# Kernel optimization log

Hardware: AMD Instinct MI355X
Metric: run time of the kernel (lower is better)

The kernel has to match this reference:

```python
import jax, jax.numpy as jnp
import numpy as np

LN_EPS = 1e-5

def setup_inputs() -> dict:
    key = jax.random.key(0)
    ks = jax.random.split(key, 6)
    N, CD, CC, CF = 500000, 64, 96, 128
    return {
        "x_detial": jax.random.normal(ks[0], (N, CD), dtype=jnp.float32),
        "x_context": jax.random.normal(ks[1], (N, CC), dtype=jnp.float32),
        "W_detial": jax.random.normal(ks[2], (CD, CF), dtype=jnp.float32) * 0.05,
        "W_context": jax.random.normal(ks[3], (CC, CF), dtype=jnp.float32) * 0.05,
        "W_gate1": jax.random.normal(ks[4], (CD + CC, CF // 2), dtype=jnp.float32) * 0.05,
        "ln_gamma": jnp.ones((CF // 2,), dtype=jnp.float32),
        "ln_beta": jnp.zeros((CF // 2,), dtype=jnp.float32),
        "W_gate2": jax.random.normal(ks[5], (CF // 2, 1), dtype=jnp.float32) * 0.05,
    }

def _layer_norm(x, gamma, beta):
    mu = jnp.mean(x, axis=-1, keepdims=True)
    var = jnp.mean(jnp.square(x - mu), axis=-1, keepdims=True)
    return (x - mu) * jax.lax.rsqrt(var + LN_EPS) * gamma + beta

def reference(x_detial, x_context, W_detial, W_context, W_gate1, ln_gamma, ln_beta, W_gate2):
    # gate path: 1x1 subm conv == per-point linear on [N, C] features
    concat = jnp.concatenate([x_detial, x_context], axis=1)        # [N, CD+CC]
    h = jnp.matmul(concat, W_gate1)                                 # [N, CF//2]
    h = jax.nn.relu(_layer_norm(h, ln_gamma, ln_beta))
    gate = jax.nn.sigmoid(jnp.matmul(h, W_gate2))                   # [N, 1]
    detail_aligned = jnp.matmul(x_detial, W_detial)                 # [N, CF]
    context_aligned = jnp.matmul(x_context, W_context)              # [N, CF]
    return (1.0 - gate) * context_aligned + gate * detail_aligned   # [N, CF]
```

## Files before the change

kernel.cpp:

```cpp
#include <hip/hip_runtime.h>
#include <hip/hip_bf16.h>
#include <math.h>


namespace {

typedef __attribute__((ext_vector_type(8))) short short8;
typedef __attribute__((ext_vector_type(4))) float f32x4;

constexpr int CD = 64, CC = 96, CH = 64, CF = 128;
constexpr int NFG1 = 20;
constexpr int NFCB = 40;
constexpr int NFRAG = NFG1 + NFCB;
constexpr int WCHUNKS = NFCB * 512 * 2 / 16;

__device__ inline short bf16_of(float f) {
  __hip_bfloat16 h = __float2bfloat16(f);
  return *reinterpret_cast<short*>(&h);
}

__global__ void convert_weights(const float* __restrict__ Wd,
                                const float* __restrict__ Wc,
                                const float* __restrict__ Wg1,
                                short* __restrict__ ws) {
  const int t = blockIdx.x * 256 + threadIdx.x;
  if (t >= 64 * NFRAG) return;
  const int frag = t >> 6, l = t & 63;
  const int cidx = l & 15, kb = l >> 4;
  float v[8];
  if (frag < NFG1) {
    const int ks = frag >> 2, nt = frag & 3;
    const int n = nt * 16 + cidx;
    #pragma unroll
    for (int j = 0; j < 8; ++j) {
      const int k = ks * 32 + (j >> 2) * 16 + kb * 4 + (j & 3);
      v[j] = Wg1[k * CH + n];
    }
  } else {
    const int f2 = frag - NFG1;
    const int ks = f2 >> 3, nt = f2 & 7;
    const int n = nt * 16 + cidx;
    #pragma unroll
    for (int j = 0; j < 8; ++j) {
      const int k = ks * 32 + (j >> 2) * 16 + kb * 4 + (j & 3);
      v[j] = (k < CD) ? Wd[k * CF + n] : Wc[(k - CD) * CF + n];
    }
  }
  short8 o;
  #pragma unroll
  for (int j = 0; j < 8; ++j) o[j] = bf16_of(v[j]);
  *reinterpret_cast<short8*>(ws + frag * 512 + l * 8) = o;
}

__global__ __launch_bounds__(512, 4)
void gate_fusion_mfma(const float* __restrict__ xd,
                      const float* __restrict__ xc,
                      const float* __restrict__ gma,
                      const float* __restrict__ bta,
                      const float* __restrict__ Wg2,
                      const short* __restrict__ wf,
                      float* __restrict__ out, int N) {
  __shared__ short wlds[NFCB * 512];

  const int tid  = threadIdx.x;
  const int lane = tid & 63;
  const int wv   = tid >> 6;
  const int r0   = blockIdx.x * 128 + wv * 16;
  const int cidx = lane & 15;
  const int kb   = lane >> 4;
  const bool active = (r0 < N);

  f32x4 buf[5][2];
  if (active) {
    const size_t row = (size_t)(r0 + cidx);
    const float* rd = xd + row * CD + kb * 4;
    const float* rc = xc + row * CC + kb * 4;
    #pragma unroll
    for (int ks = 0; ks < 5; ++ks) {
      const float* p = (ks < 2) ? (rd + ks * 32) : (rc + (ks - 2) * 32);
      buf[ks][0] = *reinterpret_cast<const f32x4*>(p);
      buf[ks][1] = *reinterpret_cast<const f32x4*>(p + 16);
    }
  }

  {
    const short* wsrc = wf + NFG1 * 512;
    #pragma unroll
    for (int it = 0; it < WCHUNKS / 512; ++it) {
      const int c = tid + it * 512;
      short8 v = *reinterpret_cast<const short8*>(wsrc + (size_t)c * 8);
      *reinterpret_cast<short8*>(&wlds[c * 8]) = v;
    }
  }

  __syncthreads();
  if (!active) return;

  float gmv[4], btv[4], w2v[4];
  #pragma unroll
  for (int nt = 0; nt < 4; ++nt) {
    const int c = nt * 16 + cidx;
    gmv[nt] = gma[c]; btv[nt] = bta[c]; w2v[nt] = Wg2[c];
  }

  short8 xf[5];
  #pragma unroll
  for (int ks = 0; ks < 5; ++ks) {
    short8 f;
    #pragma unroll
    for (int j = 0; j < 4; ++j) {
      f[j]     = bf16_of(buf[ks][0][j]);
      f[4 + j] = bf16_of(buf[ks][1][j]);
    }
    xf[ks] = f;
  }

  const f32x4 vzero = {0.f, 0.f, 0.f, 0.f};
  f32x4 acc1[4];
  #pragma unroll
  for (int nt = 0; nt < 4; ++nt) acc1[nt] = vzero;

  #pragma unroll
  for (int ks = 0; ks < 5; ++ks) {
    short8 bg[4];
    #pragma unroll
    for (int nt = 0; nt < 4; ++nt)
      bg[nt] = *reinterpret_cast<const short8*>(wf + (ks * 4 + nt) * 512 + lane * 8);
    #pragma unroll
    for (int nt = 0; nt < 4; ++nt)
      acc1[nt] = __builtin_amdgcn_mfma_f32_16x16x32_bf16(
          xf[ks], bg[nt], acc1[nt], 0, 0, 0);
  }

  float gate[4];
  {
    float s[4], q[4];
    #pragma unroll
    for (int r = 0; r < 4; ++r) {
      s[r] = 0.f; q[r] = 0.f;
      #pragma unroll
      for (int nt = 0; nt < 4; ++nt) {
        const float c = acc1[nt][r];
        s[r] += c; q[r] += c * c;
      }
    }
    #pragma unroll
    for (int m = 1; m < 16; m <<= 1)
      #pragma unroll
      for (int r = 0; r < 4; ++r) {
        s[r] += __shfl_xor(s[r], m, 64);
        q[r] += __shfl_xor(q[r], m, 64);
      }
    float p[4];
    #pragma unroll
    for (int r = 0; r < 4; ++r) {
      const float mu  = s[r] * (1.f / CH);
      const float var = q[r] * (1.f / CH) - mu * mu;
      const float rsd = rsqrtf(var + 1e-5f);
      float pp = 0.f;
      #pragma unroll
      for (int nt = 0; nt < 4; ++nt) {
        const float h = fmaxf((acc1[nt][r] - mu) * rsd * gmv[nt] + btv[nt], 0.f);
        pp += h * w2v[nt];
      }
      p[r] = pp;
    }
    #pragma unroll
    for (int m = 1; m < 16; m <<= 1)
      #pragma unroll
      for (int r = 0; r < 4; ++r) p[r] += __shfl_xor(p[r], m, 64);
    #pragma unroll
    for (int r = 0; r < 4; ++r) gate[r] = 1.f / (1.f + expf(-p[r]));
  }

  #pragma unroll
  for (int q = 0; q < 4; ++q) {
    f32x4 aD[2], aC[2];
    #pragma unroll
    for (int nt = 0; nt < 2; ++nt) { aD[nt] = vzero; aC[nt] = vzero; }

    #pragma unroll
    for (int ks = 0; ks < 5; ++ks) {
      short8 bg[2];
      #pragma unroll
      for (int nt = 0; nt < 2; ++nt)
        bg[nt] = *reinterpret_cast<const short8*>(
            &wlds[(ks * 8 + q * 2 + nt) * 512 + lane * 8]);
      if (ks < 2) {
        #pragma unroll
        for (int nt = 0; nt < 2; ++nt)
          aD[nt] = __builtin_amdgcn_mfma_f32_16x16x32_bf16(
              xf[ks], bg[nt], aD[nt], 0, 0, 0);
      } else {
        #pragma unroll
        for (int nt = 0; nt < 2; ++nt)
          aC[nt] = __builtin_amdgcn_mfma_f32_16x16x32_bf16(
              xf[ks], bg[nt], aC[nt], 0, 0, 0);
      }
    }

    {
      const size_t rowb = (size_t)r0 + kb * 4;
      #pragma unroll
      for (int nt = 0; nt < 2; ++nt) {
        #pragma unroll
        for (int r = 0; r < 4; ++r) {
          const float g = gate[r];
          const float o = fmaf(g, aD[nt][r] - aC[nt][r], aC[nt][r]);
          out[(rowb + r) * CF + (q * 2 + nt) * 16 + cidx] = o;
        }
      }
    }
  }
}

}

extern "C" void kernel_launch(void* const* d_in, const int* in_sizes, int n_in,
                              void* d_out, int out_size, void* d_ws, size_t ws_size,
                              hipStream_t stream) {
  const float* xd  = (const float*)d_in[0];
  const float* xc  = (const float*)d_in[1];
  const float* Wd  = (const float*)d_in[2];
  const float* Wc  = (const float*)d_in[3];
  const float* Wg1 = (const float*)d_in[4];
  const float* gma = (const float*)d_in[5];
  const float* bta = (const float*)d_in[6];
  const float* Wg2 = (const float*)d_in[7];
  float* out = (float*)d_out;
  short* ws  = (short*)d_ws;

  const int N = in_sizes[0] / CD;

  convert_weights<<<dim3(15), dim3(256), 0, stream>>>(Wd, Wc, Wg1, ws);

  const int nblk = (N + 127) / 128;
  gate_fusion_mfma<<<dim3(nblk), dim3(512), 0, stream>>>(
      xd, xc, gma, bta, Wg2, ws, out, N);
}
```

Baseline: 137.6 us.

## Make gate fusion kernel persistent with per-wave tile loops

Switches from one 128-row block per launch-grid entry to a fixed grid of 512 blocks, each wave looping over a contiguous range of 16-row tiles. Weight staging into LDS is amortised across many tiles instead of being repeated per small block. An opaque zero offset keeps the compiler from hoisting weight loads out of the loop, which would raise register pressure. The loop is not unrolled and input loads are not prefetched across iterations, so latency hiding now relies on occupancy. Tail handling assumes N is a multiple of 16.

Result: slower. 160.1 us (+16.3%).

```diff
diff --git a/kernel.cpp b/kernel.cpp
--- a/kernel.cpp
+++ b/kernel.cpp
@@ -52,36 +52,22 @@
   *reinterpret_cast<short8*>(ws + frag * 512 + l * 8) = o;
 }
 
-__global__ __launch_bounds__(512, 4)
+__global__ __launch_bounds__(512)
 void gate_fusion_mfma(const float* __restrict__ xd,
                       const float* __restrict__ xc,
                       const float* __restrict__ gma,
                       const float* __restrict__ bta,
                       const float* __restrict__ Wg2,
                       const short* __restrict__ wf,
-                      float* __restrict__ out, int N) {
+                      float* __restrict__ out, int nTiles, int T) {
   __shared__ short wlds[NFCB * 512];
 
   const int tid  = threadIdx.x;
   const int lane = tid & 63;
   const int wv   = tid >> 6;
-  const int r0   = blockIdx.x * 128 + wv * 16;
   const int cidx = lane & 15;
   const int kb   = lane >> 4;
-  const bool active = (r0 < N);
-
-  f32x4 buf[5][2];
-  if (active) {
-    const size_t row = (size_t)(r0 + cidx);
-    const float* rd = xd + row * CD + kb * 4;
-    const float* rc = xc + row * CC + kb * 4;
-    #pragma unroll
-    for (int ks = 0; ks < 5; ++ks) {
-      const float* p = (ks < 2) ? (rd + ks * 32) : (rc + (ks - 2) * 32);
-      buf[ks][0] = *reinterpret_cast<const f32x4*>(p);
-      buf[ks][1] = *reinterpret_cast<const f32x4*>(p + 16);
-    }
-  }
+  const int tb   = (blockIdx.x * 8 + wv) * T;
 
   {
     const short* wsrc = wf + NFG1 * 512;
@@ -92,9 +78,7 @@
       *reinterpret_cast<short8*>(&wlds[c * 8]) = v;
     }
   }
-
   __syncthreads();
-  if (!active) return;
 
   float gmv[4], btv[4], w2v[4];
   #pragma unroll
@@ -103,111 +87,136 @@
     gmv[nt] = gma[c]; btv[nt] = bta[c]; w2v[nt] = Wg2[c];
   }
 
-  short8 xf[5];
-  #pragma unroll
-  for (int ks = 0; ks < 5; ++ks) {
-    short8 f;
-    #pragma unroll
-    for (int j = 0; j < 4; ++j) {
-      f[j]     = bf16_of(buf[ks][0][j]);
-      f[4 + j] = bf16_of(buf[ks][1][j]);
-    }
-    xf[ks] = f;
-  }
-
   const f32x4 vzero = {0.f, 0.f, 0.f, 0.f};
-  f32x4 acc1[4];
-  #pragma unroll
-  for (int nt = 0; nt < 4; ++nt) acc1[nt] = vzero;
-
-  #pragma unroll
-  for (int ks = 0; ks < 5; ++ks) {
-    short8 bg[4];
-    #pragma unroll
-    for (int nt = 0; nt < 4; ++nt)
-      bg[nt] = *reinterpret_cast<const short8*>(wf + (ks * 4 + nt) * 512 + lane * 8);
-    #pragma unroll
-    for (int nt = 0; nt < 4; ++nt)
-      acc1[nt] = __builtin_amdgcn_mfma_f32_16x16x32_bf16(
-          xf[ks], bg[nt], acc1[nt], 0, 0, 0);
-  }
-
-  float gate[4];
-  {
-    float s[4], q[4];
-    #pragma unroll
-    for (int r = 0; r < 4; ++r) {
-      s[r] = 0.f; q[r] = 0.f;
-      #pragma unroll
-      for (int nt = 0; nt < 4; ++nt) {
-        const float c = acc1[nt][r];
-        s[r] += c; q[r] += c * c;
-      }
-    }
-    #pragma unroll
-    for (int m = 1; m < 16; m <<= 1)
+
+  #pragma clang loop unroll(disable)
+  for (int i = 0; i < T; ++i) {
+    const int t = tb + i;
+    if (t >= nTiles) break;
+    const int r0 = t * 16;
+
+    int lz = 0;
+    asm volatile("" : "+s"(lz));
+
+    f32x4 buf[5][2];
+    {
+      const size_t row = (size_t)(r0 + cidx);
+      const float* rd = xd + row * CD + kb * 4;
+      const float* rc = xc + row * CC + kb * 4;
+      #pragma unroll
+      for (int ks = 0; ks < 5; ++ks) {
+        const float* p = (ks < 2) ? (rd + ks * 32) : (rc + (ks - 2) * 32);
+        buf[ks][0] = *reinterpret_cast<const f32x4*>(p);
+        buf[ks][1] = *reinterpret_cast<const f32x4*>(p + 16);
+      }
+    }
+
+    short8 xf[5];
+    #pragma unroll
+    for (int ks = 0; ks < 5; ++ks) {
+      short8 f;
+      #pragma unroll
+      for (int j = 0; j < 4; ++j) {
+        f[j]     = bf16_of(buf[ks][0][j]);
+        f[4 + j] = bf16_of(buf[ks][1][j]);
+      }
+      xf[ks] = f;
+    }
+
+    f32x4 acc1[4];
+    #pragma unroll
+    for (int nt = 0; nt < 4; ++nt) acc1[nt] = vzero;
+
+    #pragma unroll
+    for (int ks = 0; ks < 5; ++ks) {
+      short8 bg[4];
+      #pragma unroll
+      for (int nt = 0; nt < 4; ++nt)
+        bg[nt] = *reinterpret_cast<const short8*>(
+            wf + (ks * 4 + nt) * 512 + lane * 8 + lz);
+      #pragma unroll
+      for (int nt = 0; nt < 4; ++nt)
+        acc1[nt] = __builtin_amdgcn_mfma_f32_16x16x32_bf16(
+            xf[ks], bg[nt], acc1[nt], 0, 0, 0);
+    }
+
+    float gate[4];
+    {
+      float s[4], q[4];
       #pragma unroll
       for (int r = 0; r < 4; ++r) {
-        s[r] += __shfl_xor(s[r], m, 64);
-        q[r] += __shfl_xor(q[r], m, 64);
-      }
-    float p[4];
-    #pragma unroll
-    for (int r = 0; r < 4; ++r) {
-      const float mu  = s[r] * (1.f / CH);
-      const float var = q[r] * (1.f / CH) - mu * mu;
-      const float rsd = rsqrtf(var + 1e-5f);
-      float pp = 0.f;
-      #pragma unroll
-      for (int nt = 0; nt < 4; ++nt) {
-        const float h = fmaxf((acc1[nt][r] - mu) * rsd * gmv[nt] + btv[nt], 0.f);
-        pp += h * w2v[nt];
-      }
-      p[r] = pp;
-    }
-    #pragma unroll
-    for (int m = 1; m < 16; m <<= 1)
-      #pragma unroll
-      for (int r = 0; r < 4; ++r) p[r] += __shfl_xor(p[r], m, 64);
-    #pragma unroll
-    for (int r = 0; r < 4; ++r) gate[r] = 1.f / (1.f + expf(-p[r]));
-  }
-
-  #pragma unroll
-  for (int q = 0; q < 4; ++q) {
-    f32x4 aD[2], aC[2];
-    #pragma unroll
-    for (int nt = 0; nt < 2; ++nt) { aD[nt] = vzero; aC[nt] = vzero; }
-
-    #pragma unroll
-    for (int ks = 0; ks < 5; ++ks) {
-      short8 bg[2];
-      #pragma unroll
-      for (int nt = 0; nt < 2; ++nt)
-        bg[nt] = *reinterpret_cast<const short8*>(
-            &wlds[(ks * 8 + q * 2 + nt) * 512 + lane * 8]);
-      if (ks < 2) {
+        s[r] = 0.f; q[r] = 0.f;
+        #pragma unroll
+        for (int nt = 0; nt < 4; ++nt) {
+          const float c = acc1[nt][r];
+          s[r] += c; q[r] += c * c;
+        }
+      }
+      #pragma unroll
+      for (int m = 1; m < 16; m <<= 1)
+        #pragma unroll
+        for (int r = 0; r < 4; ++r) {
+          s[r] += __shfl_xor(s[r], m, 64);
+          q[r] += __shfl_xor(q[r], m, 64);
+        }
+      float p[4];
+      #pragma unroll
+      for (int r = 0; r < 4; ++r) {
+        const float mu  = s[r] * (1.f / CH);
+        const float var = q[r] * (1.f / CH) - mu * mu;
+        const float rsd = rsqrtf(var + 1e-5f);
+        float pp = 0.f;
+        #pragma unroll
+        for (int nt = 0; nt < 4; ++nt) {
+          const float h = fmaxf((acc1[nt][r] - mu) * rsd * gmv[nt] + btv[nt], 0.f);
+          pp += h * w2v[nt];
+        }
+        p[r] = pp;
+      }
+      #pragma unroll
+      for (int m = 1; m < 16; m <<= 1)
+        #pragma unroll
+        for (int r = 0; r < 4; ++r) p[r] += __shfl_xor(p[r], m, 64);
+      #pragma unroll
+      for (int r = 0; r < 4; ++r) gate[r] = 1.f / (1.f + expf(-p[r]));
+    }
+
+    #pragma unroll
+    for (int q = 0; q < 4; ++q) {
+      f32x4 aD[2], aC[2];
+      #pragma unroll
+      for (int nt = 0; nt < 2; ++nt) { aD[nt] = vzero; aC[nt] = vzero; }
+
+      #pragma unroll
+      for (int ks = 0; ks < 5; ++ks) {
+        short8 bg[2];
         #pragma unroll
         for (int nt = 0; nt < 2; ++nt)
-          aD[nt] = __builtin_amdgcn_mfma_f32_16x16x32_bf16(
-              xf[ks], bg[nt], aD[nt], 0, 0, 0);
-      } else {
-        #pragma unroll
-        for (int nt = 0; nt < 2; ++nt)
-          aC[nt] = __builtin_amdgcn_mfma_f32_16x16x32_bf16(
-              xf[ks], bg[nt], aC[nt], 0, 0, 0);
-      }
-    }
-
-    {
-      const size_t rowb = (size_t)r0 + kb * 4;
-      #pragma unroll
-      for (int nt = 0; nt < 2; ++nt) {
-        #pragma unroll
-        for (int r = 0; r < 4; ++r) {
-          const float g = gate[r];
-          const float o = fmaf(g, aD[nt][r] - aC[nt][r], aC[nt][r]);
-          out[(rowb + r) * CF + (q * 2 + nt) * 16 + cidx] = o;
+          bg[nt] = *reinterpret_cast<const short8*>(
+              &wlds[(ks * 8 + q * 2 + nt) * 512 + lane * 8 + lz]);
+        if (ks < 2) {
+          #pragma unroll
+          for (int nt = 0; nt < 2; ++nt)
+            aD[nt] = __builtin_amdgcn_mfma_f32_16x16x32_bf16(
+                xf[ks], bg[nt], aD[nt], 0, 0, 0);
+        } else {
+          #pragma unroll
+          for (int nt = 0; nt < 2; ++nt)
+            aC[nt] = __builtin_amdgcn_mfma_f32_16x16x32_bf16(
+                xf[ks], bg[nt], aC[nt], 0, 0, 0);
+        }
+      }
+
+      {
+        const size_t rowb = (size_t)r0 + kb * 4;
+        #pragma unroll
+        for (int nt = 0; nt < 2; ++nt) {
+          #pragma unroll
+          for (int r = 0; r < 4; ++r) {
+            const float g = gate[r];
+            const float o = fmaf(g, aD[nt][r] - aC[nt][r], aC[nt][r]);
+            out[(rowb + r) * CF + (q * 2 + nt) * 16 + cidx] = o;
+          }
         }
       }
     }
@@ -231,10 +240,13 @@
   short* ws  = (short*)d_ws;
 
   const int N = in_sizes[0] / CD;
+  const int nTiles = N / 16;
 
   convert_weights<<<dim3(15), dim3(256), 0, stream>>>(Wd, Wc, Wg1, ws);
 
-  const int nblk = (N + 127) / 128;
+  const int nblk   = 512;
+  const int nWaves = nblk * 8;
+  const int T      = (nTiles + nWaves - 1) / nWaves;
   gate_fusion_mfma<<<dim3(nblk), dim3(512), 0, stream>>>(
-      xd, xc, gma, bta, Wg2, ws, out, N);
-}
+      xd, xc, gma, bta, Wg2, ws, out, nTiles, T);
+}
```

## Process four row tiles per wave with double-buffered inline-asm input loads

Applied to the files above, without the earlier changes.

Each wave now handles four 16-row tiles instead of one. Input loads for the next tile are issued through inline-asm global_load_dwordx4 bursts and explicit s_waitcnt, so they overlap the MFMA work on the current tile. The gate-path weights are also moved into LDS, and the weight copy is amortized over four times fewer blocks. In exchange it uses more registers (two 40-float buffers), drops the occupancy hint from the launch bounds, and assumes N is a multiple of 16.

After: 131.5 us. -4.4%, faster.

```diff
diff --git a/kernel.cpp b/kernel.cpp
--- a/kernel.cpp
+++ b/kernel.cpp
@@ -12,7 +12,7 @@
 constexpr int NFG1 = 20;
 constexpr int NFCB = 40;
 constexpr int NFRAG = NFG1 + NFCB;
-constexpr int WCHUNKS = NFCB * 512 * 2 / 16;
+constexpr int WCH_ALL = NFRAG * 512 * 2 / 16;
 
 __device__ inline short bf16_of(float f) {
   __hip_bfloat16 h = __float2bfloat16(f);
@@ -52,49 +52,51 @@
   *reinterpret_cast<short8*>(ws + frag * 512 + l * 8) = o;
 }
 
-__global__ __launch_bounds__(512, 4)
+#define BURST(p0,p1,p2,p3,p4,p5,p6,p7,p8,p9, rdp, rcp)                 \
+  asm volatile(                                                        \
+      "global_load_dwordx4 %0, %[ad], off\n\t"                         \
+      "global_load_dwordx4 %1, %[ad], off offset:64\n\t"               \
+      "global_load_dwordx4 %2, %[ad], off offset:128\n\t"              \
+      "global_load_dwordx4 %3, %[ad], off offset:192\n\t"              \
+      "global_load_dwordx4 %4, %[ac], off\n\t"                         \
+      "global_load_dwordx4 %5, %[ac], off offset:64\n\t"               \
+      "global_load_dwordx4 %6, %[ac], off offset:128\n\t"              \
+      "global_load_dwordx4 %7, %[ac], off offset:192\n\t"              \
+      "global_load_dwordx4 %8, %[ac], off offset:256\n\t"              \
+      "global_load_dwordx4 %9, %[ac], off offset:320"                  \
+      : "=&v"(p0), "=&v"(p1), "=&v"(p2), "=&v"(p3), "=&v"(p4),         \
+        "=&v"(p5), "=&v"(p6), "=&v"(p7), "=&v"(p8), "=&v"(p9)          \
+      : [ad] "v"(rdp), [ac] "v"(rcp)                                   \
+      : "memory")
+
+#define WAITB(N, p0,p1,p2,p3,p4,p5,p6,p7,p8,p9)                        \
+  asm volatile("s_waitcnt vmcnt(" #N ")"                               \
+      : "+v"(p0), "+v"(p1), "+v"(p2), "+v"(p3), "+v"(p4),              \
+        "+v"(p5), "+v"(p6), "+v"(p7), "+v"(p8), "+v"(p9)               \
+      :: "memory")
+
+__global__ __launch_bounds__(512)
 void gate_fusion_mfma(const float* __restrict__ xd,
                       const float* __restrict__ xc,
                       const float* __restrict__ gma,
                       const float* __restrict__ bta,
                       const float* __restrict__ Wg2,
                       const short* __restrict__ wf,
-                      float* __restrict__ out, int N) {
-  __shared__ short wlds[NFCB * 512];
+                      float* __restrict__ out, int nTiles) {
+  __shared__ short wlds[NFRAG * 512];
 
   const int tid  = threadIdx.x;
   const int lane = tid & 63;
   const int wv   = tid >> 6;
-  const int r0   = blockIdx.x * 128 + wv * 16;
   const int cidx = lane & 15;
   const int kb   = lane >> 4;
-  const bool active = (r0 < N);
-
-  f32x4 buf[5][2];
-  if (active) {
-    const size_t row = (size_t)(r0 + cidx);
-    const float* rd = xd + row * CD + kb * 4;
-    const float* rc = xc + row * CC + kb * 4;
-    #pragma unroll
-    for (int ks = 0; ks < 5; ++ks) {
-      const float* p = (ks < 2) ? (rd + ks * 32) : (rc + (ks - 2) * 32);
-      buf[ks][0] = *reinterpret_cast<const f32x4*>(p);
-      buf[ks][1] = *reinterpret_cast<const f32x4*>(p + 16);
-    }
+  const int tb   = (blockIdx.x * 8 + wv) * 4;
+
+  for (int c = tid; c < WCH_ALL; c += 512) {
+    short8 v = *reinterpret_cast<const short8*>(wf + (size_t)c * 8);
+    *reinterpret_cast<short8*>(&wlds[c * 8]) = v;
   }
-
-  {
-    const short* wsrc = wf + NFG1 * 512;
-    #pragma unroll
-    for (int it = 0; it < WCHUNKS / 512; ++it) {
-      const int c = tid + it * 512;
-      short8 v = *reinterpret_cast<const short8*>(wsrc + (size_t)c * 8);
-      *reinterpret_cast<short8*>(&wlds[c * 8]) = v;
-    }
-  }
-
   __syncthreads();
-  if (!active) return;
 
   float gmv[4], btv[4], w2v[4];
   #pragma unroll
@@ -103,103 +105,118 @@
     gmv[nt] = gma[c]; btv[nt] = bta[c]; w2v[nt] = Wg2[c];
   }
 
-  short8 xf[5];
-  #pragma unroll
-  for (int ks = 0; ks < 5; ++ks) {
-    short8 f;
-    #pragma unroll
-    for (int j = 0; j < 4; ++j) {
-      f[j]     = bf16_of(buf[ks][0][j]);
-      f[4 + j] = bf16_of(buf[ks][1][j]);
-    }
-    xf[ks] = f;
-  }
-
   const f32x4 vzero = {0.f, 0.f, 0.f, 0.f};
-  f32x4 acc1[4];
-  #pragma unroll
-  for (int nt = 0; nt < 4; ++nt) acc1[nt] = vzero;
-
-  #pragma unroll
-  for (int ks = 0; ks < 5; ++ks) {
-    short8 bg[4];
-    #pragma unroll
-    for (int nt = 0; nt < 4; ++nt)
-      bg[nt] = *reinterpret_cast<const short8*>(wf + (ks * 4 + nt) * 512 + lane * 8);
-    #pragma unroll
-    for (int nt = 0; nt < 4; ++nt)
-      acc1[nt] = __builtin_amdgcn_mfma_f32_16x16x32_bf16(
-          xf[ks], bg[nt], acc1[nt], 0, 0, 0);
-  }
-
-  float gate[4];
-  {
-    float s[4], q[4];
-    #pragma unroll
-    for (int r = 0; r < 4; ++r) {
-      s[r] = 0.f; q[r] = 0.f;
-      #pragma unroll
-      for (int nt = 0; nt < 4; ++nt) {
-        const float c = acc1[nt][r];
-        s[r] += c; q[r] += c * c;
-      }
-    }
-    #pragma unroll
-    for (int m = 1; m < 16; m <<= 1)
+
+  auto addrD = [&](int t) {
+    const int tc = (t < nTiles) ? t : (nTiles - 1);
+    return xd + ((size_t)tc * 16 + cidx) * CD + kb * 4;
+  };
+  auto addrC = [&](int t) {
+    const int tc = (t < nTiles) ? t : (nTiles - 1);
+    return xc + ((size_t)tc * 16 + cidx) * CC + kb * 4;
+  };
+
+  auto compute = [&](int t, const f32x4& l0, const f32x4& h0,
+                     const f32x4& l1, const f32x4& h1,
+                     const f32x4& l2, const f32x4& h2,
+                     const f32x4& l3, const f32x4& h3,
+                     const f32x4& l4, const f32x4& h4) {
+    const int r0 = t * 16;
+    const f32x4 lo[5] = {l0, l1, l2, l3, l4};
+    const f32x4 hi[5] = {h0, h1, h2, h3, h4};
+    short8 xf[5];
+    #pragma unroll
+    for (int ks = 0; ks < 5; ++ks) {
+      short8 f;
+      #pragma unroll
+      for (int j = 0; j < 4; ++j) {
+        f[j]     = bf16_of(lo[ks][j]);
+        f[4 + j] = bf16_of(hi[ks][j]);
+      }
+      xf[ks] = f;
+    }
+
+    f32x4 acc1[4];
+    #pragma unroll
+    for (int nt = 0; nt < 4; ++nt) acc1[nt] = vzero;
+    #pragma unroll
+    for (int ks = 0; ks < 5; ++ks) {
+      short8 bg[4];
+      #pragma unroll
+      for (int nt = 0; nt < 4; ++nt)
+        bg[nt] = *reinterpret_cast<const short8*>(
+            &wlds[(ks * 4 + nt) * 512 + lane * 8]);
+      #pragma unroll
+      for (int nt = 0; nt < 4; ++nt)
+        acc1[nt] = __builtin_amdgcn_mfma_f32_16x16x32_bf16(
+            xf[ks], bg[nt], acc1[nt], 0, 0, 0);
+    }
+
+    float gate[4];
+    {
+      float s[4], q[4];
       #pragma unroll
       for (int r = 0; r < 4; ++r) {
-        s[r] += __shfl_xor(s[r], m, 64);
-        q[r] += __shfl_xor(q[r], m, 64);
-      }
-    float p[4];
-    #pragma unroll
-    for (int r = 0; r < 4; ++r) {
-      const float mu  = s[r] * (1.f / CH);
-      const float var = q[r] * (1.f / CH) - mu * mu;
-      const float rsd = rsqrtf(var + 1e-5f);
-      float pp = 0.f;
-      #pragma unroll
-      for (int nt = 0; nt < 4; ++nt) {
-        const float h = fmaxf((acc1[nt][r] - mu) * rsd * gmv[nt] + btv[nt], 0.f);
-        pp += h * w2v[nt];
-      }
-      p[r] = pp;
-    }
-    #pragma unroll
-    for (int m = 1; m < 16; m <<= 1)
-      #pragma unroll
-      for (int r = 0; r < 4; ++r) p[r] += __shfl_xor(p[r], m, 64);
-    #pragma unroll
-    for (int r = 0; r < 4; ++r) gate[r] = 1.f / (1.f + expf(-p[r]));
-  }
-
-  #pragma unroll
-  for (int q = 0; q < 4; ++q) {
-    f32x4 aD[2], aC[2];
-    #pragma unroll
-    for (int nt = 0; nt < 2; ++nt) { aD[nt] = vzero; aC[nt] = vzero; }
-
-    #pragma unroll
-    for (int ks = 0; ks < 5; ++ks) {
-      short8 bg[2];
-      #pragma unroll
-      for (int nt = 0; nt < 2; ++nt)
-        bg[nt] = *reinterpret_cast<const short8*>(
-            &wlds[(ks * 8 + q * 2 + nt) * 512 + lane * 8]);
-      if (ks < 2) {
+        s[r] = 0.f; q[r] = 0.f;
+        #pragma unroll
+        for (int nt = 0; nt < 4; ++nt) {
+          const float c = acc1[nt][r];
+          s[r] += c; q[r] += c * c;
+        }
+      }
+      #pragma unroll
+      for (int m = 1; m < 16; m <<= 1)
+        #pragma unroll
+        for (int r = 0; r < 4; ++r) {
+          s[r] += __shfl_xor(s[r], m, 64);
+          q[r] += __shfl_xor(q[r], m, 64);
+        }
+      float p[4];
+      #pragma unroll
+      for (int r = 0; r < 4; ++r) {
+        const float mu  = s[r] * (1.f / CH);
+        const float var = q[r] * (1.f / CH) - mu * mu;
+        const float rsd = rsqrtf(var + 1e-5f);
+        float pp = 0.f;
+        #pragma unroll
+        for (int nt = 0; nt < 4; ++nt) {
+          const float h = fmaxf((acc1[nt][r] - mu) * rsd * gmv[nt] + btv[nt], 0.f);
+          pp += h * w2v[nt];
+        }
+        p[r] = pp;
+      }
+      #pragma unroll
+      for (int m = 1; m < 16; m <<= 1)
+        #pragma unroll
+        for (int r = 0; r < 4; ++r) p[r] += __shfl_xor(p[r], m, 64);
+      #pragma unroll
+      for (int r = 0; r < 4; ++r) gate[r] = 1.f / (1.f + expf(-p[r]));
+    }
+
+    #pragma unroll
+    for (int q = 0; q < 4; ++q) {
+      f32x4 aD[2], aC[2];
+      #pragma unroll
+      for (int nt = 0; nt < 2; ++nt) { aD[nt] = vzero; aC[nt] = vzero; }
+      #pragma unroll
+      for (int ks = 0; ks < 5; ++ks) {
+        short8 bg[2];
         #pragma unroll
         for (int nt = 0; nt < 2; ++nt)
-          aD[nt] = __builtin_amdgcn_mfma_f32_16x16x32_bf16(
-              xf[ks], bg[nt], aD[nt], 0, 0, 0);
-      } else {
-        #pragma unroll
-        for (int nt = 0; nt < 2; ++nt)
-          aC[nt] = __builtin_amdgcn_mfma_f32_16x16x32_bf16(
-              xf[ks], bg[nt], aC[nt], 0, 0, 0);
-      }
-    }
-
-    {
+          bg[nt] = *reinterpret_cast<const short8*>(
+              &wlds[(NFG1 + ks * 8 + q * 2 + nt) * 512 + lane * 8]);
+        if (ks < 2) {
+          #pragma unroll
+          for (int nt = 0; nt < 2; ++nt)
+            aD[nt] = __builtin_amdgcn_mfma_f32_16x16x32_bf16(
+                xf[ks], bg[nt], aD[nt], 0, 0, 0);
+        } else {
+          #pragma unroll
+          for (int nt = 0; nt < 2; ++nt)
+            aC[nt] = __builtin_amdgcn_mfma_f32_16x16x32_bf16(
+                xf[ks], bg[nt], aC[nt], 0, 0, 0);
+        }
+      }
       const size_t rowb = (size_t)r0 + kb * 4;
       #pragma unroll
       for (int nt = 0; nt < 2; ++nt) {
@@ -211,7 +228,27 @@
         }
       }
     }
-  }
+  };
+
+  f32x4 a0, a1, a2, a3, a4, a5, a6, a7, a8, a9;
+  f32x4 b0, b1, b2, b3, b4, b5, b6, b7, b8, b9;
+
+  BURST(a0,a1,a2,a3,a4,a5,a6,a7,a8,a9, addrD(tb),     addrC(tb));
+  BURST(b0,b1,b2,b3,b4,b5,b6,b7,b8,b9, addrD(tb + 1), addrC(tb + 1));
+
+  WAITB(10, a0,a1,a2,a3,a4,a5,a6,a7,a8,a9);
+  if (tb < nTiles)     compute(tb,     a0,a1, a2,a3, a4,a5, a6,a7, a8,a9);
+
+  BURST(a0,a1,a2,a3,a4,a5,a6,a7,a8,a9, addrD(tb + 2), addrC(tb + 2));
+  WAITB(10, b0,b1,b2,b3,b4,b5,b6,b7,b8,b9);
+  if (tb + 1 < nTiles) compute(tb + 1, b0,b1, b2,b3, b4,b5, b6,b7, b8,b9);
+
+  BURST(b0,b1,b2,b3,b4,b5,b6,b7,b8,b9, addrD(tb + 3), addrC(tb + 3));
+  WAITB(10, a0,a1,a2,a3,a4,a5,a6,a7,a8,a9);
+  if (tb + 2 < nTiles) compute(tb + 2, a0,a1, a2,a3, a4,a5, a6,a7, a8,a9);
+
+  WAITB(0, b0,b1,b2,b3,b4,b5,b6,b7,b8,b9);
+  if (tb + 3 < nTiles) compute(tb + 3, b0,b1, b2,b3, b4,b5, b6,b7, b8,b9);
 }
 
 }
@@ -231,10 +268,12 @@
   short* ws  = (short*)d_ws;
 
   const int N = in_sizes[0] / CD;
+  const int nTiles = N / 16;
 
   convert_weights<<<dim3(15), dim3(256), 0, stream>>>(Wd, Wc, Wg1, ws);
 
-  const int nblk = (N + 127) / 128;
+  const int tilesPerBlock = 8 * 4;
+  const int nblk = (nTiles + tilesPerBlock - 1) / tilesPerBlock;
   gate_fusion_mfma<<<dim3(nblk), dim3(512), 0, stream>>>(
-      xd, xc, gma, bta, Wg2, ws, out, N);
-}
+      xd, xc, gma, bta, Wg2, ws, out, nTiles);
+}
```
